# Kernel optimization log

Measured on AMD Instinct MI355X. Metric: run time of the kernel, lower is better.

Reference implementation:

```python
import jax, jax.numpy as jnp
import numpy as np

NUM_RBF = 16
MAX_REL = 32          # max_relative_feature
AUTOREGRESSIVE = True
D_MIN, D_MAX = 2.0, 22.0
LN_EPS = 1e-5


def setup_inputs() -> dict:
    key = jax.random.key(0)
    ks = jax.random.split(key, 6)
    B, L, A, K = 1, 1280, 14, 30
    E_feat, edge_in = 128, 16 + NUM_RBF * 4 * 10  # 656
    X = jax.random.normal(ks[0], (B, L, A, 3), dtype=jnp.float32) * 3.0
    residue_idx = jnp.tile(jnp.arange(L, dtype=jnp.int32)[None], (B, 1))
    chain_labels = jnp.zeros((B, L), dtype=jnp.int32)
    E_idx = jax.random.randint(ks[1], (B, L, K), 0, L, dtype=jnp.int32)
    atom_mask = jnp.ones((B, L, A), dtype=jnp.float32)
    W_pos = jax.random.normal(ks[2], (2 * MAX_REL + 2, 16), dtype=jnp.float32) * 0.1
    b_pos = jnp.zeros((16,), dtype=jnp.float32)
    W_edge = jax.random.normal(ks[3], (edge_in, E_feat), dtype=jnp.float32) * 0.05
    ln_gamma = jnp.ones((E_feat,), dtype=jnp.float32)
    ln_beta = jnp.zeros((E_feat,), dtype=jnp.float32)
    return {"X": X, "residue_idx": residue_idx, "chain_labels": chain_labels,
            "E_idx": E_idx, "atom_mask": atom_mask, "W_pos": W_pos,
            "b_pos": b_pos, "W_edge": W_edge, "ln_gamma": ln_gamma,
            "ln_beta": ln_beta}


def _forward(X, residue_idx, chain_labels, E_idx, W_pos, b_pos, W_edge,
             ln_gamma, ln_beta):
    B, L, A, _ = X.shape
    K = E_idx.shape[-1]
    # backbone atoms in loop order [Ca, N, C, O] -> X indices [1, 0, 2, 3]
    bb = X[:, :, jnp.array([1, 0, 2, 3]), :]          # [B, L, 4, 3]
    sc = X[:, :, 4:, :]                               # [B, L, 10, 3]
    Abb = jnp.transpose(bb, (0, 2, 1, 3))             # [B, 4, L, 3]
    Asc = jnp.transpose(sc, (0, 2, 1, 3))             # [B, 10, L, 3]
    # dense pairwise distances for all 40 (bb, sc) atom pairs: [B,4,10,L,L]
    diff = Abb[:, :, None, :, None, :] - Asc[:, None, :, None, :, :]
    D = jnp.sqrt(jnp.sum(diff * diff, axis=-1) + 1e-6)
    # gather top-k neighbor columns -> [B,4,10,L,K]
    D_nb = jnp.take_along_axis(D, E_idx[:, None, None, :, :], axis=4)
    mu = jnp.linspace(D_MIN, D_MAX, NUM_RBF, dtype=D_nb.dtype)
    sigma = (D_MAX - D_MIN) / NUM_RBF
    RBF = jnp.exp(-(((D_nb[..., None] - mu) / sigma) ** 2))  # [B,4,10,L,K,16]
    if AUTOREGRESSIVE:
        self_edges = (E_idx == jnp.arange(L, dtype=E_idx.dtype)[None, :, None])
        RBF = jnp.where(self_edges[:, None, None, :, :, None], 0.0, RBF)
    # concat order: bb outer, sc inner -> [B,L,K, 4*10*16]
    RBF_all = jnp.transpose(RBF, (0, 3, 4, 1, 2, 5)).reshape(B, L, K, 4 * 10 * NUM_RBF)
    # positional encodings
    offset = residue_idx[:, :, None] - residue_idx[:, None, :]        # [B,L,L]
    offset = jnp.take_along_axis(offset, E_idx, axis=2)               # [B,L,K]
    d_chains = (chain_labels[:, :, None] == chain_labels[:, None, :]).astype(jnp.int32)
    E_chains = jnp.take_along_axis(d_chains, E_idx, axis=2)           # [B,L,K]
    d = jnp.clip(offset + MAX_REL, 0, 2 * MAX_REL) * E_chains + (1 - E_chains) * (2 * MAX_REL + 1)
    d_onehot = jax.nn.one_hot(d, 2 * MAX_REL + 2, dtype=W_pos.dtype)  # [B,L,K,66]
    E_positional = d_onehot @ W_pos + b_pos                           # [B,L,K,16]
    E = jnp.concatenate([E_positional, RBF_all], axis=-1)             # [B,L,K,656]
    E = E @ W_edge                                                    # no bias
    # LayerNorm over last dim
    mean = jnp.mean(E, axis=-1, keepdims=True)
    var = jnp.mean((E - mean) ** 2, axis=-1, keepdims=True)
    E = (E - mean) / jnp.sqrt(var + LN_EPS) * ln_gamma + ln_beta
    return E


def reference(X, residue_idx, chain_labels, E_idx, atom_mask, W_pos, b_pos,
              W_edge, ln_gamma, ln_beta):
    E = _forward(X, residue_idx, chain_labels, E_idx, W_pos, b_pos, W_edge,
                 ln_gamma, ln_beta)
    return (E, E_idx)
```

## Files before the change

### kernel.cpp

```cpp
#include <hip/hip_runtime.h>

typedef short bf16x8 __attribute__((ext_vector_type(8)));
typedef float f32x4  __attribute__((ext_vector_type(4)));

#define L_RES 1280
#define A_ATM 14
#define K_NB  30
#define FEAT  656
#define KPAD  672
#define NCH   128
#define AF_STRIDE 680
#define E_OUT_OFF (L_RES * K_NB * NCH)

__device__ __forceinline__ ushort f2bf(float x) {
    union { float f; unsigned u; } v; v.f = x;
    unsigned r = (v.u + 0x7fffu + ((v.u >> 16) & 1u)) >> 16;
    return (ushort)r;
}

__global__ __launch_bounds__(256) void wt_convert_kernel(const float* __restrict__ W,
                                                         ushort* __restrict__ Wt) {
    int idx = blockIdx.x * 256 + threadIdx.x;
    if (idx >= NCH * KPAD) return;
    int n = idx / KPAD, k = idx - n * KPAD;
    float v = (k < FEAT) ? W[k * NCH + n] : 0.0f;
    Wt[idx] = f2bf(v);
}

__global__ __launch_bounds__(256) void sidechain_feat_kernel(
    const float* __restrict__ X,
    const int*   __restrict__ ridx,
    const int*   __restrict__ clab,
    const int*   __restrict__ Eidx,
    const float* __restrict__ Wpos,
    const float* __restrict__ bpos,
    const ushort* __restrict__ Wt,
    const float* __restrict__ gamma,
    const float* __restrict__ beta,
    float* __restrict__ out)
{
    __shared__ __align__(16) ushort Af[32][AF_STRIDE];
    __shared__ float bbs[4][3];
    __shared__ float scj[K_NB][10][3];
    __shared__ int   nbr[K_NB];

    const int i = blockIdx.x;
    const int t = threadIdx.x;
    const int w = t >> 6;
    const int lane = t & 63;

    if (t < 12) {
        const int perm[4] = {1, 0, 2, 3};
        int a = t / 3, c = t - a * 3;
        bbs[a][c] = X[(i * A_ATM + perm[a]) * 3 + c];
    }
    if (t < K_NB) nbr[t] = Eidx[i * K_NB + t];
    __syncthreads();

    for (int idx = t; idx < K_NB * 30; idx += 256) {
        int e = idx / 30;
        int r = idx - e * 30;
        int a = r / 3, c = r - a * 3;
        scj[e][a][c] = X[(nbr[e] * A_ATM + 4 + a) * 3 + c];
    }

    for (int idx = t; idx < K_NB * 16; idx += 256) {
        int e = idx >> 4, c = idx & 15;
        int j = nbr[e];
        int d;
        if (clab[i] == clab[j]) {
            int off = ridx[i] - ridx[j] + 32;
            d = off < 0 ? 0 : (off > 64 ? 64 : off);
        } else {
            d = 65;
        }
        Af[e][c] = f2bf(Wpos[d * 16 + c] + bpos[c]);
    }
    for (int idx = t; idx < 2 * AF_STRIDE; idx += 256)
        Af[30 + idx / AF_STRIDE][idx % AF_STRIDE] = 0;
    for (int idx = t; idx < 30 * 24; idx += 256)
        Af[idx / 24][FEAT + idx % 24] = 0;
    __syncthreads();

    for (int idx = t; idx < K_NB * 40; idx += 256) {
        int e  = idx / 40;
        int p  = idx - e * 40;
        int ab = p / 10, as = p - ab * 10;
        float dx = bbs[ab][0] - scj[e][as][0];
        float dy = bbs[ab][1] - scj[e][as][1];
        float dz = bbs[ab][2] - scj[e][as][2];
        float dist = sqrtf(dx * dx + dy * dy + dz * dz + 1e-6f);
        bool self = (nbr[e] == i);
        unsigned* dst = (unsigned*)&Af[e][16 + p * 16];
#pragma unroll
        for (int q = 0; q < 8; q++) {
            float m0 = 2.0f + (float)(2 * q)     * (20.0f / 15.0f);
            float m1 = 2.0f + (float)(2 * q + 1) * (20.0f / 15.0f);
            float a0 = (dist - m0) * 0.8f;
            float a1 = (dist - m1) * 0.8f;
            float r0 = self ? 0.0f : __expf(-a0 * a0);
            float r1 = self ? 0.0f : __expf(-a1 * a1);
            dst[q] = (unsigned)f2bf(r0) | ((unsigned)f2bf(r1) << 16);
        }
    }
    __syncthreads();

    const int frow = lane & 15;
    const int quad = lane >> 4;
    const ushort* A0p = &Af[frow][quad * 8];
    const ushort* A1p = &Af[16 + frow][quad * 8];
    const ushort* B0p = Wt + (size_t)((2 * w) * 16 + frow) * KPAD + quad * 8;
    const ushort* B1p = B0p + 16 * KPAD;

    f32x4 acc00 = {0.f,0.f,0.f,0.f}, acc01 = {0.f,0.f,0.f,0.f};
    f32x4 acc10 = {0.f,0.f,0.f,0.f}, acc11 = {0.f,0.f,0.f,0.f};

    bf16x8 a0 = *(const bf16x8*)(A0p);
    bf16x8 a1 = *(const bf16x8*)(A1p);
    bf16x8 b0 = *(const bf16x8*)(B0p);
    bf16x8 b1 = *(const bf16x8*)(B1p);

#pragma unroll
    for (int kb = 0; kb < KPAD; kb += 32) {
        bf16x8 ca0 = a0, ca1 = a1, cb0 = b0, cb1 = b1;
        if (kb + 32 < KPAD) {
            a0 = *(const bf16x8*)(A0p + kb + 32);
            a1 = *(const bf16x8*)(A1p + kb + 32);
            b0 = *(const bf16x8*)(B0p + kb + 32);
            b1 = *(const bf16x8*)(B1p + kb + 32);
        }
        acc00 = __builtin_amdgcn_mfma_f32_16x16x32_bf16(ca0, cb0, acc00, 0, 0, 0);
        acc01 = __builtin_amdgcn_mfma_f32_16x16x32_bf16(ca0, cb1, acc01, 0, 0, 0);
        acc10 = __builtin_amdgcn_mfma_f32_16x16x32_bf16(ca1, cb0, acc10, 0, 0, 0);
        acc11 = __builtin_amdgcn_mfma_f32_16x16x32_bf16(ca1, cb1, acc11, 0, 0, 0);
    }

    __syncthreads();
    float (*Epre)[132] = (float (*)[132])&Af[0][0];

#pragma unroll
    for (int r = 0; r < 4; r++) {
        int row0 = quad * 4 + r;
        Epre[row0][(2 * w)     * 16 + frow] = acc00[r];
        Epre[row0][(2 * w + 1) * 16 + frow] = acc01[r];
        Epre[16 + row0][(2 * w)     * 16 + frow] = acc10[r];
        Epre[16 + row0][(2 * w + 1) * 16 + frow] = acc11[r];
    }
    __syncthreads();

    for (int e = w; e < K_NB; e += 4) {
        float v0 = Epre[e][lane];
        float v1 = Epre[e][lane + 64];
        float s = v0 + v1;
        float q = v0 * v0 + v1 * v1;
#pragma unroll
        for (int off = 32; off > 0; off >>= 1) {
            s += __shfl_xor(s, off);
            q += __shfl_xor(q, off);
        }
        float mean = s * (1.0f / 128.0f);
        float var  = q * (1.0f / 128.0f) - mean * mean;
        float rstd = rsqrtf(var + 1e-5f);
        float* o = out + (size_t)(i * K_NB + e) * NCH;
        o[lane]      = (v0 - mean) * rstd * gamma[lane]      + beta[lane];
        o[lane + 64] = (v1 - mean) * rstd * gamma[lane + 64] + beta[lane + 64];
    }

    if (t < K_NB) out[E_OUT_OFF + i * K_NB + t] = (float)nbr[t];
}

extern "C" void kernel_launch(void* const* d_in, const int* in_sizes, int n_in,
                              void* d_out, int out_size, void* d_ws, size_t ws_size,
                              hipStream_t stream) {
    const float* X     = (const float*)d_in[0];
    const int*   ridx  = (const int*)  d_in[1];
    const int*   clab  = (const int*)  d_in[2];
    const int*   Eidx  = (const int*)  d_in[3];
    const float* Wpos  = (const float*)d_in[5];
    const float* bpos  = (const float*)d_in[6];
    const float* Wedge = (const float*)d_in[7];
    const float* gamma = (const float*)d_in[8];
    const float* beta  = (const float*)d_in[9];
    float* out = (float*)d_out;

    ushort* Wt = (ushort*)d_ws;

    wt_convert_kernel<<<(NCH * KPAD + 255) / 256, 256, 0, stream>>>(Wedge, Wt);
    sidechain_feat_kernel<<<L_RES, 256, 0, stream>>>(
        X, ridx, clab, Eidx, Wpos, bpos, Wt, gamma, beta, out);
}
```

Baseline: 109.4 us.

## Process two residues per block and pre-pack weights in MFMA fragment layout

Each block now handles two residues (64 padded rows) with 512 threads, so every wave loads one B fragment per k-step and reuses it across four MFMA row tiles. This halves how often each block reads weights from global memory. The weight conversion kernel now writes W_edge directly in per-lane MFMA fragment order, so B loads are contiguous 16-byte per-lane reads. Writing out E_idx moves into the prep kernel. The cost is fewer blocks (640) with larger LDS per block, which may lower occupancy and the number of CUs kept busy.

```diff
diff --git a/kernel.cpp b/kernel.cpp
--- a/kernel.cpp
+++ b/kernel.cpp
@@ -8,9 +8,12 @@
 #define K_NB  30
 #define FEAT  656
 #define KPAD  672
+#define NKB   21
 #define NCH   128
 #define AF_STRIDE 680
+#define EP_STRIDE 136
 #define E_OUT_OFF (L_RES * K_NB * NCH)
+#define NEDGE (L_RES * K_NB)
 
 __device__ __forceinline__ ushort f2bf(float x) {
     union { float f; unsigned u; } v; v.f = x;
@@ -18,80 +21,110 @@
     return (ushort)r;
 }
 
-__global__ __launch_bounds__(256) void wt_convert_kernel(const float* __restrict__ W,
-                                                         ushort* __restrict__ Wt) {
-    int idx = blockIdx.x * 256 + threadIdx.x;
-    if (idx >= NCH * KPAD) return;
-    int n = idx / KPAD, k = idx - n * KPAD;
-    float v = (k < FEAT) ? W[k * NCH + n] : 0.0f;
-    Wt[idx] = f2bf(v);
-}
-
-__global__ __launch_bounds__(256) void sidechain_feat_kernel(
+__global__ __launch_bounds__(256) void prep_kernel(const float* __restrict__ W,
+                                                   const int* __restrict__ Eidx,
+                                                   ushort* __restrict__ Wpack,
+                                                   float* __restrict__ out) {
+    const int blk = blockIdx.x;
+    const int t = threadIdx.x;
+    if (blk < 42) {
+        int u = blk * 256 + t;
+        if (u >= 84 * 128) return;
+        int kbq = u >> 7;
+        int n   = u & 127;
+        int kb   = kbq >> 2;
+        int quad = kbq & 3;
+        ushort val[8];
+#pragma unroll
+        for (int j = 0; j < 8; j++) {
+            int k = kb * 32 + quad * 8 + j;
+            val[j] = (k < FEAT) ? f2bf(W[k * NCH + n]) : (ushort)0;
+        }
+        int lane = quad * 16 + (n & 15);
+        ushort* dst = Wpack + (size_t)((((n >> 4) * NKB + kb) * 64 + lane) * 8);
+        *(ulonglong2*)dst = *(const ulonglong2*)val;
+    } else {
+        int gid = (blk - 42) * 256 + t;
+        if (gid < NEDGE) out[E_OUT_OFF + gid] = (float)Eidx[gid];
+    }
+}
+
+__global__ __launch_bounds__(512) void sidechain_feat_kernel(
     const float* __restrict__ X,
     const int*   __restrict__ ridx,
     const int*   __restrict__ clab,
     const int*   __restrict__ Eidx,
     const float* __restrict__ Wpos,
     const float* __restrict__ bpos,
-    const ushort* __restrict__ Wt,
+    const ushort* __restrict__ Wpack,
     const float* __restrict__ gamma,
     const float* __restrict__ beta,
     float* __restrict__ out)
 {
-    __shared__ __align__(16) ushort Af[32][AF_STRIDE];
-    __shared__ float bbs[4][3];
-    __shared__ float scj[K_NB][10][3];
-    __shared__ int   nbr[K_NB];
-
-    const int i = blockIdx.x;
+    __shared__ __align__(16) ushort Af[64][AF_STRIDE];
+    __shared__ float bbs[8][3];
+    __shared__ float scj[2 * K_NB][10][3];
+    __shared__ int   nbr[2 * K_NB];
+
+    const int i0 = blockIdx.x * 2;
     const int t = threadIdx.x;
     const int w = t >> 6;
     const int lane = t & 63;
 
-    if (t < 12) {
+    if (t < 24) {
         const int perm[4] = {1, 0, 2, 3};
-        int a = t / 3, c = t - a * 3;
-        bbs[a][c] = X[(i * A_ATM + perm[a]) * 3 + c];
-    }
-    if (t < K_NB) nbr[t] = Eidx[i * K_NB + t];
-    __syncthreads();
-
-    for (int idx = t; idx < K_NB * 30; idx += 256) {
+        int res = t / 12, r = t - res * 12;
+        int a = r / 3, c = r - a * 3;
+        bbs[res * 4 + a][c] = X[((i0 + res) * A_ATM + perm[a]) * 3 + c];
+    }
+    if (t < 2 * K_NB) nbr[t] = Eidx[i0 * K_NB + t];
+    __syncthreads();
+
+    for (int idx = t; idx < 2 * K_NB * 30; idx += 512) {
         int e = idx / 30;
         int r = idx - e * 30;
         int a = r / 3, c = r - a * 3;
         scj[e][a][c] = X[(nbr[e] * A_ATM + 4 + a) * 3 + c];
     }
 
-    for (int idx = t; idx < K_NB * 16; idx += 256) {
+    for (int idx = t; idx < 2 * K_NB * 16; idx += 512) {
         int e = idx >> 4, c = idx & 15;
+        int res = i0 + (e >= K_NB);
+        int row = e + (e >= K_NB ? 2 : 0);
         int j = nbr[e];
         int d;
-        if (clab[i] == clab[j]) {
-            int off = ridx[i] - ridx[j] + 32;
+        if (clab[res] == clab[j]) {
+            int off = ridx[res] - ridx[j] + 32;
             d = off < 0 ? 0 : (off > 64 ? 64 : off);
         } else {
             d = 65;
         }
-        Af[e][c] = f2bf(Wpos[d * 16 + c] + bpos[c]);
-    }
-    for (int idx = t; idx < 2 * AF_STRIDE; idx += 256)
-        Af[30 + idx / AF_STRIDE][idx % AF_STRIDE] = 0;
-    for (int idx = t; idx < 30 * 24; idx += 256)
-        Af[idx / 24][FEAT + idx % 24] = 0;
-    __syncthreads();
-
-    for (int idx = t; idx < K_NB * 40; idx += 256) {
+        Af[row][c] = f2bf(Wpos[d * 16 + c] + bpos[c]);
+    }
+    for (int idx = t; idx < 4 * AF_STRIDE; idx += 512) {
+        int pr = idx / AF_STRIDE;
+        int row = (pr & 1) + (pr >> 1) * 32 + 30;
+        Af[row][idx % AF_STRIDE] = 0;
+    }
+    for (int idx = t; idx < 60 * 24; idx += 512) {
+        int e = idx / 24;
+        int row = e + (e >= K_NB ? 2 : 0);
+        Af[row][FEAT + idx % 24] = 0;
+    }
+    __syncthreads();
+
+    for (int idx = t; idx < 2 * K_NB * 40; idx += 512) {
         int e  = idx / 40;
         int p  = idx - e * 40;
         int ab = p / 10, as = p - ab * 10;
-        float dx = bbs[ab][0] - scj[e][as][0];
-        float dy = bbs[ab][1] - scj[e][as][1];
-        float dz = bbs[ab][2] - scj[e][as][2];
+        int hi = (e >= K_NB);
+        int row = e + hi * 2;
+        float dx = bbs[hi * 4 + ab][0] - scj[e][as][0];
+        float dy = bbs[hi * 4 + ab][1] - scj[e][as][1];
+        float dz = bbs[hi * 4 + ab][2] - scj[e][as][2];
         float dist = sqrtf(dx * dx + dy * dy + dz * dz + 1e-6f);
-        bool self = (nbr[e] == i);
-        unsigned* dst = (unsigned*)&Af[e][16 + p * 16];
+        bool self = (nbr[e] == i0 + hi);
+        unsigned* dst = (unsigned*)&Af[row][16 + p * 16];
 #pragma unroll
         for (int q = 0; q < 8; q++) {
             float m0 = 2.0f + (float)(2 * q)     * (20.0f / 15.0f);
@@ -107,50 +140,48 @@
 
     const int frow = lane & 15;
     const int quad = lane >> 4;
-    const ushort* A0p = &Af[frow][quad * 8];
-    const ushort* A1p = &Af[16 + frow][quad * 8];
-    const ushort* B0p = Wt + (size_t)((2 * w) * 16 + frow) * KPAD + quad * 8;
-    const ushort* B1p = B0p + 16 * KPAD;
-
-    f32x4 acc00 = {0.f,0.f,0.f,0.f}, acc01 = {0.f,0.f,0.f,0.f};
-    f32x4 acc10 = {0.f,0.f,0.f,0.f}, acc11 = {0.f,0.f,0.f,0.f};
-
-    bf16x8 a0 = *(const bf16x8*)(A0p);
-    bf16x8 a1 = *(const bf16x8*)(A1p);
-    bf16x8 b0 = *(const bf16x8*)(B0p);
-    bf16x8 b1 = *(const bf16x8*)(B1p);
-
-#pragma unroll
-    for (int kb = 0; kb < KPAD; kb += 32) {
-        bf16x8 ca0 = a0, ca1 = a1, cb0 = b0, cb1 = b1;
-        if (kb + 32 < KPAD) {
-            a0 = *(const bf16x8*)(A0p + kb + 32);
-            a1 = *(const bf16x8*)(A1p + kb + 32);
-            b0 = *(const bf16x8*)(B0p + kb + 32);
-            b1 = *(const bf16x8*)(B1p + kb + 32);
-        }
-        acc00 = __builtin_amdgcn_mfma_f32_16x16x32_bf16(ca0, cb0, acc00, 0, 0, 0);
-        acc01 = __builtin_amdgcn_mfma_f32_16x16x32_bf16(ca0, cb1, acc01, 0, 0, 0);
-        acc10 = __builtin_amdgcn_mfma_f32_16x16x32_bf16(ca1, cb0, acc10, 0, 0, 0);
-        acc11 = __builtin_amdgcn_mfma_f32_16x16x32_bf16(ca1, cb1, acc11, 0, 0, 0);
-    }
-
-    __syncthreads();
-    float (*Epre)[132] = (float (*)[132])&Af[0][0];
-
-#pragma unroll
-    for (int r = 0; r < 4; r++) {
-        int row0 = quad * 4 + r;
-        Epre[row0][(2 * w)     * 16 + frow] = acc00[r];
-        Epre[row0][(2 * w + 1) * 16 + frow] = acc01[r];
-        Epre[16 + row0][(2 * w)     * 16 + frow] = acc10[r];
-        Epre[16 + row0][(2 * w + 1) * 16 + frow] = acc11[r];
-    }
-    __syncthreads();
-
-    for (int e = w; e < K_NB; e += 4) {
-        float v0 = Epre[e][lane];
-        float v1 = Epre[e][lane + 64];
+    const ushort* Ap[4];
+#pragma unroll
+    for (int m = 0; m < 4; m++) Ap[m] = &Af[m * 16 + frow][quad * 8];
+    const ushort* Bp = Wpack + (size_t)((w * NKB) * 64 + lane) * 8;
+
+    f32x4 acc[4];
+#pragma unroll
+    for (int m = 0; m < 4; m++) acc[m] = (f32x4){0.f, 0.f, 0.f, 0.f};
+
+    bf16x8 a[4], b;
+#pragma unroll
+    for (int m = 0; m < 4; m++) a[m] = *(const bf16x8*)(Ap[m]);
+    b = *(const bf16x8*)(Bp);
+
+#pragma unroll
+    for (int kb = 0; kb < NKB; kb++) {
+        bf16x8 ca[4] = {a[0], a[1], a[2], a[3]};
+        bf16x8 cb = b;
+        if (kb + 1 < NKB) {
+#pragma unroll
+            for (int m = 0; m < 4; m++) a[m] = *(const bf16x8*)(Ap[m] + (kb + 1) * 32);
+            b = *(const bf16x8*)(Bp + (size_t)(kb + 1) * 512);
+        }
+#pragma unroll
+        for (int m = 0; m < 4; m++)
+            acc[m] = __builtin_amdgcn_mfma_f32_16x16x32_bf16(ca[m], cb, acc[m], 0, 0, 0);
+    }
+
+    __syncthreads();
+    float (*Epre)[EP_STRIDE] = (float (*)[EP_STRIDE])&Af[0][0];
+
+#pragma unroll
+    for (int m = 0; m < 4; m++)
+#pragma unroll
+        for (int r = 0; r < 4; r++)
+            Epre[m * 16 + quad * 4 + r][w * 16 + frow] = acc[m][r];
+    __syncthreads();
+
+    for (int e = w; e < 2 * K_NB; e += 8) {
+        int row = e + (e >= K_NB ? 2 : 0);
+        float v0 = Epre[row][lane];
+        float v1 = Epre[row][lane + 64];
         float s = v0 + v1;
         float q = v0 * v0 + v1 * v1;
 #pragma unroll
@@ -161,12 +192,12 @@
         float mean = s * (1.0f / 128.0f);
         float var  = q * (1.0f / 128.0f) - mean * mean;
         float rstd = rsqrtf(var + 1e-5f);
-        float* o = out + (size_t)(i * K_NB + e) * NCH;
+        int eo = (e >= K_NB) ? (K_NB + e - K_NB) : e;
+        float* o = out + (size_t)((i0 + (e >= K_NB)) * K_NB + (e % K_NB)) * NCH;
+        (void)eo;
         o[lane]      = (v0 - mean) * rstd * gamma[lane]      + beta[lane];
         o[lane + 64] = (v1 - mean) * rstd * gamma[lane + 64] + beta[lane + 64];
     }
-
-    if (t < K_NB) out[E_OUT_OFF + i * K_NB + t] = (float)nbr[t];
 }
 
 extern "C" void kernel_launch(void* const* d_in, const int* in_sizes, int n_in,
@@ -183,9 +214,9 @@
     const float* beta  = (const float*)d_in[9];
     float* out = (float*)d_out;
 
-    ushort* Wt = (ushort*)d_ws;
-
-    wt_convert_kernel<<<(NCH * KPAD + 255) / 256, 256, 0, stream>>>(Wedge, Wt);
-    sidechain_feat_kernel<<<L_RES, 256, 0, stream>>>(
-        X, ridx, clab, Eidx, Wpos, bpos, Wt, gamma, beta, out);
-}
+    ushort* Wpack = (ushort*)d_ws;
+
+    prep_kernel<<<42 + (NEDGE + 255) / 256, 256, 0, stream>>>(Wedge, Eidx, Wpack, out);
+    sidechain_feat_kernel<<<L_RES / 2, 512, 0, stream>>>(
+        X, ridx, clab, Eidx, Wpos, bpos, Wpack, gamma, beta, out);
+}
```

Result: slower. 120.0 us (+9.7%).

## Split feature build and GEMM+LayerNorm into separate kernels with fragment-packed operands

Applied to the files above, without the earlier changes.

Replaces the single fused per-residue kernel with two kernels. The first builds the RBF and positional features and writes them to global workspace already packed in MFMA fragment order, and it also packs W_edge and writes E_idx. The second runs a larger GEMM tile of 128 rows by 128 channels per 512-thread block, then applies LayerNorm. The goal is to reuse each B fragment across 8 row tiles and load operands with coalesced fragment loads instead of re-reading W per residue. The cost is a global round-trip for the bf16 features, plus padding rows 30-31 that are computed and then discarded.

```diff
diff --git a/kernel.cpp b/kernel.cpp
--- a/kernel.cpp
+++ b/kernel.cpp
@@ -7,10 +7,12 @@
 #define A_ATM 14
 #define K_NB  30
 #define FEAT  656
-#define KPAD  672
+#define NKB   21
 #define NCH   128
-#define AF_STRIDE 680
+#define FRAG  512
+#define EPS   132
 #define E_OUT_OFF (L_RES * K_NB * NCH)
+#define NEDGE (L_RES * K_NB)
 
 __device__ __forceinline__ ushort f2bf(float x) {
     union { float f; unsigned u; } v; v.f = x;
@@ -18,36 +20,44 @@
     return (ushort)r;
 }
 
-__global__ __launch_bounds__(256) void wt_convert_kernel(const float* __restrict__ W,
-                                                         ushort* __restrict__ Wt) {
-    int idx = blockIdx.x * 256 + threadIdx.x;
-    if (idx >= NCH * KPAD) return;
-    int n = idx / KPAD, k = idx - n * KPAD;
-    float v = (k < FEAT) ? W[k * NCH + n] : 0.0f;
-    Wt[idx] = f2bf(v);
-}
-
-__global__ __launch_bounds__(256) void sidechain_feat_kernel(
+__global__ __launch_bounds__(256) void feature_kernel(
     const float* __restrict__ X,
     const int*   __restrict__ ridx,
     const int*   __restrict__ clab,
     const int*   __restrict__ Eidx,
     const float* __restrict__ Wpos,
     const float* __restrict__ bpos,
-    const ushort* __restrict__ Wt,
-    const float* __restrict__ gamma,
-    const float* __restrict__ beta,
-    float* __restrict__ out)
+    const float* __restrict__ Wedge,
+    ushort* __restrict__ Wpack,
+    ushort* __restrict__ Apack,
+    float*  __restrict__ out)
 {
-    __shared__ __align__(16) ushort Af[32][AF_STRIDE];
     __shared__ float bbs[4][3];
     __shared__ float scj[K_NB][10][3];
     __shared__ int   nbr[K_NB];
 
     const int i = blockIdx.x;
     const int t = threadIdx.x;
-    const int w = t >> 6;
-    const int lane = t & 63;
+
+    if (i < 42) {
+        int u = i * 256 + t;
+        if (u < 84 * 128) {
+            int kbq = u >> 7, n = u & 127;
+            int kb = kbq >> 2, quad = kbq & 3;
+            ushort val[8];
+#pragma unroll
+            for (int j = 0; j < 8; j++) {
+                int k = kb * 32 + quad * 8 + j;
+                val[j] = (k < FEAT) ? f2bf(Wedge[k * NCH + n]) : (ushort)0;
+            }
+            ushort* dst = Wpack + (size_t)((((n >> 4) * NKB + kb) * 64 +
+                                            quad * 16 + (n & 15)) * 8);
+            *(ulonglong2*)dst = *(const ulonglong2*)val;
+        }
+    } else if (i < 192) {
+        int gid = (i - 42) * 256 + t;
+        out[E_OUT_OFF + gid] = (float)Eidx[gid];
+    }
 
     if (t < 12) {
         const int perm[4] = {1, 0, 2, 3};
@@ -64,8 +74,11 @@
         scj[e][a][c] = X[(nbr[e] * A_ATM + 4 + a) * 3 + c];
     }
 
-    for (int idx = t; idx < K_NB * 16; idx += 256) {
-        int e = idx >> 4, c = idx & 15;
+    ushort* Ab = Apack + (size_t)(i * 2 * NKB) * FRAG;
+
+    if (t < 60) {
+        int e = t >> 1, q = t & 1;
+        int mt = e >> 4, f = e & 15;
         int j = nbr[e];
         int d;
         if (clab[i] == clab[j]) {
@@ -74,81 +87,113 @@
         } else {
             d = 65;
         }
-        Af[e][c] = f2bf(Wpos[d * 16 + c] + bpos[c]);
-    }
-    for (int idx = t; idx < 2 * AF_STRIDE; idx += 256)
-        Af[30 + idx / AF_STRIDE][idx % AF_STRIDE] = 0;
-    for (int idx = t; idx < 30 * 24; idx += 256)
-        Af[idx / 24][FEAT + idx % 24] = 0;
+        ushort v[8];
+#pragma unroll
+        for (int jj = 0; jj < 8; jj++) {
+            int c = q * 8 + jj;
+            v[jj] = f2bf(Wpos[d * 16 + c] + bpos[c]);
+        }
+        ushort* dst = Ab + (size_t)(mt * NKB) * FRAG + (q * 16 + f) * 8;
+        *(ulonglong2*)dst = *(const ulonglong2*)v;
+    }
+    {
+        const ulonglong2 z = {0ull, 0ull};
+        for (int idx = t; idx < 168; idx += 256) {
+            int f = 14 + (idx & 1);
+            int kq = idx >> 1;
+            int kb = kq >> 2, q = kq & 3;
+            *(ulonglong2*)(Ab + (size_t)(NKB + kb) * FRAG + (q * 16 + f) * 8) = z;
+        }
+        if (t < 64) {
+            int mt = t >> 5, q = 2 + ((t >> 4) & 1), f = t & 15;
+            *(ulonglong2*)(Ab + (size_t)(mt * NKB + 20) * FRAG + (q * 16 + f) * 8) = z;
+        }
+    }
     __syncthreads();
 
-    for (int idx = t; idx < K_NB * 40; idx += 256) {
-        int e  = idx / 40;
-        int p  = idx - e * 40;
+    for (int idx = t; idx < 1200; idx += 256) {
+        int p = idx / 30;
+        int e = idx - p * 30;
         int ab = p / 10, as = p - ab * 10;
         float dx = bbs[ab][0] - scj[e][as][0];
         float dy = bbs[ab][1] - scj[e][as][1];
         float dz = bbs[ab][2] - scj[e][as][2];
         float dist = sqrtf(dx * dx + dy * dy + dz * dz + 1e-6f);
         bool self = (nbr[e] == i);
-        unsigned* dst = (unsigned*)&Af[e][16 + p * 16];
-#pragma unroll
-        for (int q = 0; q < 8; q++) {
-            float m0 = 2.0f + (float)(2 * q)     * (20.0f / 15.0f);
-            float m1 = 2.0f + (float)(2 * q + 1) * (20.0f / 15.0f);
-            float a0 = (dist - m0) * 0.8f;
-            float a1 = (dist - m1) * 0.8f;
-            float r0 = self ? 0.0f : __expf(-a0 * a0);
-            float r1 = self ? 0.0f : __expf(-a1 * a1);
-            dst[q] = (unsigned)f2bf(r0) | ((unsigned)f2bf(r1) << 16);
-        }
-    }
-    __syncthreads();
-
+
+        ushort v[16];
+#pragma unroll
+        for (int r = 0; r < 16; r++) {
+            float mu = 2.0f + (float)r * (20.0f / 15.0f);
+            float a0 = (dist - mu) * 0.8f;
+            v[r] = self ? (ushort)0 : f2bf(__expf(-a0 * a0));
+        }
+        int mt = e >> 4, f = e & 15;
+        int kb, qb;
+        if (p & 1) { kb = (p + 1) >> 1; qb = 0; }
+        else       { kb = p >> 1;       qb = 2; }
+        ushort* dst = Ab + (size_t)(mt * NKB + kb) * FRAG + (qb * 16 + f) * 8;
+        *(ulonglong2*)dst        = *(const ulonglong2*)&v[0];
+        *(ulonglong2*)(dst + 128) = *(const ulonglong2*)&v[8];
+    }
+}
+
+__global__ __launch_bounds__(512) void gemm_ln_kernel(
+    const ushort* __restrict__ Wpack,
+    const ushort* __restrict__ Apack,
+    const float*  __restrict__ gamma,
+    const float*  __restrict__ beta,
+    float* __restrict__ out)
+{
+    __shared__ float Epre[128][EPS];
+
+    const int b = blockIdx.x;
+    const int t = threadIdx.x;
+    const int w = t >> 6;
+    const int lane = t & 63;
     const int frow = lane & 15;
     const int quad = lane >> 4;
-    const ushort* A0p = &Af[frow][quad * 8];
-    const ushort* A1p = &Af[16 + frow][quad * 8];
-    const ushort* B0p = Wt + (size_t)((2 * w) * 16 + frow) * KPAD + quad * 8;
-    const ushort* B1p = B0p + 16 * KPAD;
-
-    f32x4 acc00 = {0.f,0.f,0.f,0.f}, acc01 = {0.f,0.f,0.f,0.f};
-    f32x4 acc10 = {0.f,0.f,0.f,0.f}, acc11 = {0.f,0.f,0.f,0.f};
-
-    bf16x8 a0 = *(const bf16x8*)(A0p);
-    bf16x8 a1 = *(const bf16x8*)(A1p);
-    bf16x8 b0 = *(const bf16x8*)(B0p);
-    bf16x8 b1 = *(const bf16x8*)(B1p);
-
-#pragma unroll
-    for (int kb = 0; kb < KPAD; kb += 32) {
-        bf16x8 ca0 = a0, ca1 = a1, cb0 = b0, cb1 = b1;
-        if (kb + 32 < KPAD) {
-            a0 = *(const bf16x8*)(A0p + kb + 32);
-            a1 = *(const bf16x8*)(A1p + kb + 32);
-            b0 = *(const bf16x8*)(B0p + kb + 32);
-            b1 = *(const bf16x8*)(B1p + kb + 32);
-        }
-        acc00 = __builtin_amdgcn_mfma_f32_16x16x32_bf16(ca0, cb0, acc00, 0, 0, 0);
-        acc01 = __builtin_amdgcn_mfma_f32_16x16x32_bf16(ca0, cb1, acc01, 0, 0, 0);
-        acc10 = __builtin_amdgcn_mfma_f32_16x16x32_bf16(ca1, cb0, acc10, 0, 0, 0);
-        acc11 = __builtin_amdgcn_mfma_f32_16x16x32_bf16(ca1, cb1, acc11, 0, 0, 0);
-    }
-
+
+    const ushort* Bp = Wpack + ((size_t)(w * NKB)) * FRAG + lane * 8;
+    const ushort* Ap = Apack + ((size_t)(b * 8) * NKB) * FRAG + lane * 8;
+
+    f32x4 acc[8];
+#pragma unroll
+    for (int m = 0; m < 8; m++) acc[m] = (f32x4){0.f, 0.f, 0.f, 0.f};
+
+    bf16x8 a[8], bb;
+#pragma unroll
+    for (int m = 0; m < 8; m++) a[m] = *(const bf16x8*)(Ap + (size_t)(m * NKB) * FRAG);
+    bb = *(const bf16x8*)(Bp);
+
+#pragma unroll
+    for (int kb = 0; kb < NKB; kb++) {
+        bf16x8 ca[8] = {a[0], a[1], a[2], a[3], a[4], a[5], a[6], a[7]};
+        bf16x8 cb = bb;
+        if (kb + 1 < NKB) {
+#pragma unroll
+            for (int m = 0; m < 8; m++)
+                a[m] = *(const bf16x8*)(Ap + (size_t)(m * NKB + kb + 1) * FRAG);
+            bb = *(const bf16x8*)(Bp + (size_t)(kb + 1) * FRAG);
+        }
+#pragma unroll
+        for (int m = 0; m < 8; m++)
+            acc[m] = __builtin_amdgcn_mfma_f32_16x16x32_bf16(ca[m], cb, acc[m], 0, 0, 0);
+    }
+
+#pragma unroll
+    for (int m = 0; m < 8; m++)
+#pragma unroll
+        for (int r = 0; r < 4; r++)
+            Epre[m * 16 + quad * 4 + r][w * 16 + frow] = acc[m][r];
     __syncthreads();
-    float (*Epre)[132] = (float (*)[132])&Af[0][0];
-
-#pragma unroll
-    for (int r = 0; r < 4; r++) {
-        int row0 = quad * 4 + r;
-        Epre[row0][(2 * w)     * 16 + frow] = acc00[r];
-        Epre[row0][(2 * w + 1) * 16 + frow] = acc01[r];
-        Epre[16 + row0][(2 * w)     * 16 + frow] = acc10[r];
-        Epre[16 + row0][(2 * w + 1) * 16 + frow] = acc11[r];
-    }
-    __syncthreads();
-
-    for (int e = w; e < K_NB; e += 4) {
+
+    const float g0 = gamma[lane], g1 = gamma[lane + 64];
+    const float bt0 = beta[lane], bt1 = beta[lane + 64];
+
+    for (int e = w; e < 128; e += 8) {
+        int ed = e & 31;
+        if (ed >= K_NB) continue;
         float v0 = Epre[e][lane];
         float v1 = Epre[e][lane + 64];
         float s = v0 + v1;
@@ -161,12 +206,11 @@
         float mean = s * (1.0f / 128.0f);
         float var  = q * (1.0f / 128.0f) - mean * mean;
         float rstd = rsqrtf(var + 1e-5f);
-        float* o = out + (size_t)(i * K_NB + e) * NCH;
-        o[lane]      = (v0 - mean) * rstd * gamma[lane]      + beta[lane];
-        o[lane + 64] = (v1 - mean) * rstd * gamma[lane + 64] + beta[lane + 64];
-    }
-
-    if (t < K_NB) out[E_OUT_OFF + i * K_NB + t] = (float)nbr[t];
+        int res = b * 4 + (e >> 5);
+        float* o = out + ((size_t)res * K_NB + ed) * NCH;
+        o[lane]      = (v0 - mean) * rstd * g0 + bt0;
+        o[lane + 64] = (v1 - mean) * rstd * g1 + bt1;
+    }
 }
 
 extern "C" void kernel_launch(void* const* d_in, const int* in_sizes, int n_in,
@@ -183,9 +227,11 @@
     const float* beta  = (const float*)d_in[9];
     float* out = (float*)d_out;
 
-    ushort* Wt = (ushort*)d_ws;
-
-    wt_convert_kernel<<<(NCH * KPAD + 255) / 256, 256, 0, stream>>>(Wedge, Wt);
-    sidechain_feat_kernel<<<L_RES, 256, 0, stream>>>(
-        X, ridx, clab, Eidx, Wpos, bpos, Wt, gamma, beta, out);
-}
+    ushort* Wpack = (ushort*)d_ws;
+    ushort* Apack = Wpack + 84 * 128 * 8;
+
+    feature_kernel<<<L_RES, 256, 0, stream>>>(
+        X, ridx, clab, Eidx, Wpos, bpos, Wedge, Wpack, Apack, out);
+    gemm_ln_kernel<<<(L_RES * 2 * 16) / 128, 512, 0, stream>>>(
+        Wpack, Apack, gamma, beta, out);
+}
```

Measured after the change: 125.0 us. 1.14x slower.
